# Performance work log

Hardware: AMD Instinct MI355X
Metric: run time of the kernel (lower is better)

## Reference

```python
import jax, jax.numpy as jnp
import numpy as np

N = 2048
E = 32768
IN_CH = 512
HID = 64
HEADS = 4
OUT_CH = 64
NUM_HOPS = 2
BETA = 0.5
NEG_SLOPE = 0.2
LN_EPS = 1e-5


def setup_inputs() -> dict:
    key = jax.random.key(0)
    ks = jax.random.split(key, 12)
    x = jax.random.normal(ks[0], (N, IN_CH), jnp.float32)
    edge_index = jax.random.randint(ks[1], (2, E), 0, N, dtype=jnp.int32)
    g = lambda k, shape, fan_in: jax.random.normal(k, shape, jnp.float32) * (1.0 / np.sqrt(fan_in))
    return {
        'x': x,
        'edge_index': edge_index,
        'l1_lin_w': g(ks[2], (NUM_HOPS, IN_CH, HEADS * HID), IN_CH),
        'l1_att_src': g(ks[3], (NUM_HOPS, HEADS, HID), HID),
        'l1_att_dst': g(ks[4], (NUM_HOPS, HEADS, HID), HID),
        'l1_hop_att': jnp.ones((NUM_HOPS,), jnp.float32),
        'l1_bias': g(ks[5], (HEADS * HID,), HEADS * HID),
        'l2_lin_w': g(ks[6], (NUM_HOPS, HEADS * HID, OUT_CH), HEADS * HID),
        'l2_att_src': g(ks[7], (NUM_HOPS, 1, OUT_CH), OUT_CH),
        'l2_att_dst': g(ks[8], (NUM_HOPS, 1, OUT_CH), OUT_CH),
        'l2_hop_att': jnp.ones((NUM_HOPS,), jnp.float32),
        'l2_res_w': g(ks[9], (HEADS * HID, OUT_CH), HEADS * HID),
        'l2_ln_scale': jnp.ones((OUT_CH,), jnp.float32),
        'l2_ln_bias': jnp.zeros((OUT_CH,), jnp.float32),
        'l2_bias': g(ks[10], (OUT_CH,), OUT_CH),
    }


def _leaky(v):
    return jnp.where(v >= 0, v, NEG_SLOPE * v)


def _masked_softmax_src(score, mask):
    # PyG softmax(alpha, edge_index[1]): normalize over src (axis 0) per dst column.
    s = jnp.where(mask[:, :, None], score, -jnp.inf)
    s = s - jnp.max(s, axis=0, keepdims=True)  # diag always valid -> finite max
    e = jnp.exp(s)
    return e / jnp.sum(e, axis=0, keepdims=True)


def _mgat_conv(x, A, motif, lin_w, att_src, att_dst, hop_att, heads, out_ch, concat,
               res_w=None, ln_scale=None, ln_bias=None, bias=None, residual=False):
    n = x.shape[0]
    hop_w = jax.nn.softmax(hop_att)
    eye = jnp.eye(n, dtype=bool)
    out = 0.0
    A_pow = A  # adj^(hop+1)
    for hop in range(NUM_HOPS):
        mask = (A_pow > 0) | eye  # remove_self_loops + add_self_loops -> diag always in
        hop_x = (x @ lin_w[hop]).reshape(n, heads, out_ch)
        s_src = jnp.einsum('nhc,hc->nh', hop_x, att_src[hop])
        s_dst = jnp.einsum('nhc,hc->nh', hop_x, att_dst[hop])
        score = s_src[:, None, :] + s_dst[None, :, :]  # [src, dst, h]
        a_first = _masked_softmax_src(_leaky(score), mask)
        a_motif = _masked_softmax_src(_leaky(score * motif[:, :, None]), mask)
        alpha = BETA * a_first + (1.0 - BETA) * a_motif
        hop_out = jnp.einsum('sdh,shc->dhc', alpha, hop_x)  # scatter-add at dst
        out = out + hop_w[hop] * hop_out
        A_pow = A_pow @ A
    if concat:
        out = out.reshape(n, heads * out_ch)
    else:
        out = out.mean(axis=1)
    if residual:
        res = x @ res_w if res_w is not None else x
        out = out + res
        mu = jnp.mean(out, axis=-1, keepdims=True)
        var = jnp.mean((out - mu) ** 2, axis=-1, keepdims=True)
        out = (out - mu) / jnp.sqrt(var + LN_EPS) * ln_scale + ln_bias
    if bias is not None:
        out = out + bias
    return out


def reference(x, edge_index, l1_lin_w, l1_att_src, l1_att_dst, l1_hop_att, l1_bias,
              l2_lin_w, l2_att_src, l2_att_dst, l2_hop_att, l2_res_w,
              l2_ln_scale, l2_ln_bias, l2_bias):
    n = x.shape[0]
    A = jnp.zeros((n, n), x.dtype).at[edge_index[0], edge_index[1]].set(1.0)
    motif = A @ A @ A
    motif = motif / jnp.maximum(motif.sum(axis=-1, keepdims=True), 1.0)
    h = _mgat_conv(x, A, motif, l1_lin_w, l1_att_src, l1_att_dst, l1_hop_att,
                   heads=HEADS, out_ch=HID, concat=True, bias=l1_bias, residual=False)
    h = jax.nn.elu(h)  # dropout p in eval mode -> identity
    out = _mgat_conv(h, A, motif, l2_lin_w, l2_att_src, l2_att_dst, l2_hop_att,
                     heads=1, out_ch=OUT_CH, concat=False,
                     res_w=l2_res_w, ln_scale=l2_ln_scale, ln_bias=l2_ln_bias,
                     bias=l2_bias, residual=True)
    return out
```

## Files before the change

kernel.cpp:

```cpp
#include <hip/hip_runtime.h>

namespace {

constexpr int kN = 2048;
constexpr int kWords = kN / 64;
constexpr int kC1 = 256;
constexpr int kC2 = 64;
constexpr int kIN = 512;
constexpr float kNegSlope = 0.2f;
constexpr float kLnEps = 1e-5f;

__device__ __forceinline__ float leakyf(float v) {
  return v >= 0.f ? v : kNegSlope * v;
}
__device__ __forceinline__ void onl(float& m, float& l, float v) {
  if (v > m) { l = l * __expf(m - v) + 1.f; m = v; }
  else       { l += __expf(v - m); }
}
__device__ __forceinline__ void mergeml(float& M, float& L, float m, float l) {
  if (m > M) { L = L * __expf(M - m) + l; M = m; }
  else       { L += l * __expf(m - M); }
}

__global__ void build_bits(const int* __restrict__ ei, int E,
                           unsigned long long* rowbits, unsigned long long* colbitsT) {
  int e = blockIdx.x * 256 + threadIdx.x;
  if (e >= E) return;
  int s = ei[e], d = ei[E + e];
  atomicOr(&rowbits[(size_t)s * kWords + (d >> 6)], 1ull << (d & 63));
  atomicOr(&colbitsT[(size_t)(s >> 6) * kN + d], 1ull << (s & 63));
}

__global__ __launch_bounds__(256) void a2_tiled(
    const unsigned long long* __restrict__ rowbits,
    const unsigned long long* __restrict__ colbitsT,
    unsigned short* __restrict__ A2,
    unsigned long long* __restrict__ colbits2T) {
  int bx = blockIdx.x, by = blockIdx.y;
  int t = threadIdx.x;
  __shared__ unsigned long long rb[64][33];
  __shared__ unsigned long long cb[32][64];
  __shared__ unsigned long long cw[64];
  int s0 = by * 64, d0 = bx * 64;
  for (int i = t; i < 64 * 32; i += 256) {
    int ss = i >> 5, w = i & 31;
    rb[ss][w] = rowbits[(size_t)(s0 + ss) * kWords + w];
  }
  for (int i = t; i < 32 * 64; i += 256) {
    int w = i >> 6, dd = i & 63;
    cb[w][dd] = colbitsT[(size_t)w * kN + d0 + dd];
  }
  if (t < 64) cw[t] = 0ull;
  __syncthreads();
  int tx = t & 15, ty4 = (t >> 4) * 4;
  int acc[4][4] = {};
#pragma unroll 4
  for (int w = 0; w < 32; ++w) {
    unsigned long long r0 = rb[ty4 + 0][w], r1 = rb[ty4 + 1][w];
    unsigned long long r2 = rb[ty4 + 2][w], r3 = rb[ty4 + 3][w];
    unsigned long long c0 = cb[w][tx], c1 = cb[w][tx + 16];
    unsigned long long c2 = cb[w][tx + 32], c3 = cb[w][tx + 48];
    acc[0][0] += __popcll(r0 & c0); acc[0][1] += __popcll(r0 & c1);
    acc[0][2] += __popcll(r0 & c2); acc[0][3] += __popcll(r0 & c3);
    acc[1][0] += __popcll(r1 & c0); acc[1][1] += __popcll(r1 & c1);
    acc[1][2] += __popcll(r1 & c2); acc[1][3] += __popcll(r1 & c3);
    acc[2][0] += __popcll(r2 & c0); acc[2][1] += __popcll(r2 & c1);
    acc[2][2] += __popcll(r2 & c2); acc[2][3] += __popcll(r2 & c3);
    acc[3][0] += __popcll(r3 & c0); acc[3][1] += __popcll(r3 & c1);
    acc[3][2] += __popcll(r3 & c2); acc[3][3] += __popcll(r3 & c3);
  }
#pragma unroll
  for (int i = 0; i < 4; ++i)
#pragma unroll
    for (int j = 0; j < 4; ++j)
      A2[(size_t)(s0 + ty4 + i) * kN + d0 + tx + 16 * j] = (unsigned short)acc[i][j];
#pragma unroll
  for (int j = 0; j < 4; ++j) {
    unsigned long long m = 0;
#pragma unroll
    for (int i = 0; i < 4; ++i)
      if (acc[i][j]) m |= 1ull << (ty4 + i);
    if (m) atomicOr(&cw[tx + 16 * j], m);
  }
  __syncthreads();
  if (t < 64) colbits2T[(size_t)by * kN + d0 + t] = cw[t];
}

__global__ __launch_bounds__(256) void a3_dense(
    const unsigned long long* __restrict__ rowbits,
    const unsigned short* __restrict__ A2,
    unsigned short* __restrict__ a3u,
    float* __restrict__ invr) {
  int s = blockIdx.x;
  int t = threadIdx.x;
  int lane = t & 63;
  __shared__ unsigned short jl[kN];
  __shared__ int jtot_s;
  __shared__ float redv[4];
  if (t < 64) {
    unsigned long long word = (lane < kWords) ? rowbits[(size_t)s * kWords + lane] : 0ull;
    int c = __popcll(word);
    int inc = c;
    for (int o = 1; o < 64; o <<= 1) { int v = __shfl_up(inc, o); if (lane >= o) inc += v; }
    if (lane == 63) jtot_s = inc;
    int off = inc - c;
    int base = lane * 64;
    while (word) {
      int b = __builtin_ctzll(word);
      word &= word - 1;
      jl[off++] = (unsigned short)(base + b);
    }
  }
  __syncthreads();
  int jtot = jtot_s;
  const uint4* a2v = reinterpret_cast<const uint4*>(A2);
  uint4 acc = make_uint4(0u, 0u, 0u, 0u);
  int ji = 0;
  for (; ji + 4 <= jtot; ji += 4) {
    uint4 v0 = a2v[(size_t)jl[ji + 0] * 256 + t];
    uint4 v1 = a2v[(size_t)jl[ji + 1] * 256 + t];
    uint4 v2 = a2v[(size_t)jl[ji + 2] * 256 + t];
    uint4 v3 = a2v[(size_t)jl[ji + 3] * 256 + t];
    acc.x += v0.x + v1.x + v2.x + v3.x;
    acc.y += v0.y + v1.y + v2.y + v3.y;
    acc.z += v0.z + v1.z + v2.z + v3.z;
    acc.w += v0.w + v1.w + v2.w + v3.w;
  }
  for (; ji < jtot; ++ji) {
    uint4 v = a2v[(size_t)jl[ji] * 256 + t];
    acc.x += v.x; acc.y += v.y; acc.z += v.z; acc.w += v.w;
  }
  reinterpret_cast<uint4*>(a3u)[(size_t)s * 256 + t] = acc;
  float tot = (float)((acc.x & 0xffffu) + (acc.x >> 16) +
                      (acc.y & 0xffffu) + (acc.y >> 16) +
                      (acc.z & 0xffffu) + (acc.z >> 16) +
                      (acc.w & 0xffffu) + (acc.w >> 16));
  for (int o = 32; o; o >>= 1) tot += __shfl_xor(tot, o);
  if (lane == 0) redv[t >> 6] = tot;
  __syncthreads();
  if (t == 0)
    invr[s] = 1.f / fmaxf(redv[0] + redv[1] + redv[2] + redv[3], 1.f);
}

__global__ __launch_bounds__(256) void transpose_motif(
    const unsigned short* __restrict__ a3u, const float* __restrict__ invr,
    float* __restrict__ motifT) {
  __shared__ float tile[64][65];
  __shared__ float invs[64];
  int d0 = blockIdx.x * 64, s0 = blockIdx.y * 64;
  int t = threadIdx.x;
  int tx = t & 63, ty = t >> 6;
  if (t < 64) invs[t] = invr[s0 + t];
  __syncthreads();
#pragma unroll
  for (int i = 0; i < 64; i += 4)
    tile[ty + i][tx] = (float)a3u[(size_t)(s0 + ty + i) * kN + d0 + tx] * invs[ty + i];
  __syncthreads();
#pragma unroll
  for (int i = 0; i < 64; i += 4)
    motifT[(size_t)(d0 + ty + i) * kN + s0 + tx] = tile[tx][ty + i];
}

__global__ __launch_bounds__(256) void gemm1(
    const float* __restrict__ x, const float* __restrict__ l1w,
    float* __restrict__ hx1,
    const float* __restrict__ l1as, const float* __restrict__ l1ad,
    float* __restrict__ ss1, float* __restrict__ sd1) {
  int hop = blockIdx.z;
  int row0 = blockIdx.y * 32, col0 = blockIdx.x * 64;
  const float* B = l1w + (size_t)hop * kIN * kC1;
  float* Cz = hx1 + (size_t)hop * kN * kC1;
  __shared__ float As[16][34];
  __shared__ float Bs[16][65];
  int t = threadIdx.x;
  int tx = t & 15, ty = t >> 4;
  float acc[2][4] = {};
  for (int k0 = 0; k0 < kIN; k0 += 16) {
    if (t < 128) {
      int m = t >> 2, kk = (t & 3) * 4;
      float4 va = *reinterpret_cast<const float4*>(x + (size_t)(row0 + m) * kIN + k0 + kk);
      As[kk + 0][m] = va.x; As[kk + 1][m] = va.y;
      As[kk + 2][m] = va.z; As[kk + 3][m] = va.w;
    }
    {
      int kb = t >> 4, nb = (t & 15) * 4;
      float4 vb = *reinterpret_cast<const float4*>(B + (size_t)(k0 + kb) * kC1 + col0 + nb);
      Bs[kb][nb + 0] = vb.x; Bs[kb][nb + 1] = vb.y;
      Bs[kb][nb + 2] = vb.z; Bs[kb][nb + 3] = vb.w;
    }
    __syncthreads();
#pragma unroll
    for (int kk2 = 0; kk2 < 16; ++kk2) {
      float a0 = As[kk2][ty * 2 + 0];
      float a1 = As[kk2][ty * 2 + 1];
      float b[4];
#pragma unroll
      for (int j = 0; j < 4; ++j) b[j] = Bs[kk2][tx * 4 + j];
#pragma unroll
      for (int j = 0; j < 4; ++j) {
        acc[0][j] += a0 * b[j];
        acc[1][j] += a1 * b[j];
      }
    }
    __syncthreads();
  }
#pragma unroll
  for (int i = 0; i < 2; ++i)
#pragma unroll
    for (int j = 0; j < 4; ++j)
      Cz[(size_t)(row0 + ty * 2 + i) * kC1 + col0 + tx * 4 + j] = acc[i][j];
  int h = col0 >> 6;
  float as_[4], ad_[4];
#pragma unroll
  for (int j = 0; j < 4; ++j) {
    as_[j] = l1as[hop * kC1 + col0 + tx * 4 + j];
    ad_[j] = l1ad[hop * kC1 + col0 + tx * 4 + j];
  }
#pragma unroll
  for (int i = 0; i < 2; ++i) {
    float ps = acc[i][0] * as_[0] + acc[i][1] * as_[1] +
               acc[i][2] * as_[2] + acc[i][3] * as_[3];
    float pd = acc[i][0] * ad_[0] + acc[i][1] * ad_[1] +
               acc[i][2] * ad_[2] + acc[i][3] * ad_[3];
#pragma unroll
    for (int o = 1; o < 16; o <<= 1) {
      ps += __shfl_xor(ps, o);
      pd += __shfl_xor(pd, o);
    }
    if (tx == 0) {
      int n = row0 + ty * 2 + i;
      ss1[((size_t)hop * kN + n) * 4 + h] = ps;
      sd1[((size_t)hop * kN + n) * 4 + h] = pd;
    }
  }
}

__global__ __launch_bounds__(256) void gemm2(
    const float* __restrict__ A, const float* __restrict__ l2w,
    const float* __restrict__ l2rw, float* __restrict__ C,
    const float* __restrict__ attS, const float* __restrict__ attD,
    float* __restrict__ ssO, float* __restrict__ sdO) {
  int z = blockIdx.z;
  const float* B = (z < 2) ? l2w + (size_t)z * kC1 * kC2 : l2rw;
  float* Cz = C + (size_t)z * kN * kC2;
  __shared__ float As[16][34];
  __shared__ float Bs[16][65];
  int t = threadIdx.x;
  int tx = t & 15, ty = t >> 4;
  int row0 = blockIdx.y * 16;
  float acc[4] = {};
  for (int k0 = 0; k0 < kC1; k0 += 16) {
    if (t < 64) {
      int m = t >> 2, kk = (t & 3) * 4;
      float4 va = *reinterpret_cast<const float4*>(A + (size_t)(row0 + m) * kC1 + k0 + kk);
      As[kk + 0][m] = va.x; As[kk + 1][m] = va.y;
      As[kk + 2][m] = va.z; As[kk + 3][m] = va.w;
    }
    {
      int kb = t >> 4, nb = (t & 15) * 4;
      float4 vb = *reinterpret_cast<const float4*>(B + (size_t)(k0 + kb) * kC2 + nb);
      Bs[kb][nb + 0] = vb.x; Bs[kb][nb + 1] = vb.y;
      Bs[kb][nb + 2] = vb.z; Bs[kb][nb + 3] = vb.w;
    }
    __syncthreads();
#pragma unroll
    for (int kk2 = 0; kk2 < 16; ++kk2) {
      float a = As[kk2][ty];
#pragma unroll
      for (int j = 0; j < 4; ++j) acc[j] += a * Bs[kk2][tx * 4 + j];
    }
    __syncthreads();
  }
#pragma unroll
  for (int j = 0; j < 4; ++j)
    Cz[(size_t)(row0 + ty) * kC2 + tx * 4 + j] = acc[j];
  if (z < 2) {
    float as_[4], ad_[4];
#pragma unroll
    for (int j = 0; j < 4; ++j) {
      as_[j] = attS[z * kC2 + tx * 4 + j];
      ad_[j] = attD[z * kC2 + tx * 4 + j];
    }
    float ps = acc[0] * as_[0] + acc[1] * as_[1] + acc[2] * as_[2] + acc[3] * as_[3];
    float pd = acc[0] * ad_[0] + acc[1] * ad_[1] + acc[2] * ad_[2] + acc[3] * ad_[3];
#pragma unroll
    for (int o = 1; o < 16; o <<= 1) {
      ps += __shfl_xor(ps, o);
      pd += __shfl_xor(pd, o);
    }
    if (tx == 0) {
      int n = row0 + ty;
      ssO[(size_t)z * kN + n] = ps;
      sdO[(size_t)z * kN + n] = pd;
    }
  }
}

__global__ __launch_bounds__(256) void agg_l1(
    const float* __restrict__ hx,
    const float* __restrict__ ssrc,
    const float* __restrict__ sdst,
    const float* __restrict__ motifT,
    const unsigned long long* __restrict__ colbitsT,
    const unsigned long long* __restrict__ colbits2T,
    const float* __restrict__ hop_att,
    const float* __restrict__ bias,
    float* __restrict__ hbuf) {
  int d = blockIdx.x;
  int t = threadIdx.x;
  int lane = t & 63;
  int h = t >> 6;
  int cq = lane;
  int hq = cq >> 4;
  __shared__ unsigned short slist[kN];
  __shared__ float mrow[kN];
  __shared__ float w_lds[64 * 4];
  __shared__ int s_total;
  __shared__ float4 red4[4][64];
  {
    const float4* mp = reinterpret_cast<const float4*>(motifT + (size_t)d * kN);
    float4* mr = reinterpret_cast<float4*>(mrow);
    mr[t] = mp[t];
    mr[t + 256] = mp[t + 256];
  }
  float a0 = hop_att[0], a1 = hop_att[1];
  float mxa = fmaxf(a0, a1);
  float e0 = __expf(a0 - mxa), e1 = __expf(a1 - mxa);
  float wh0 = e0 / (e0 + e1), wh1 = e1 / (e0 + e1);
  float4 acc4 = make_float4(0.f, 0.f, 0.f, 0.f);
  for (int hop = 0; hop < 2; ++hop) {
    const unsigned long long* cm = hop ? colbits2T : colbitsT;
    if (t < 64) {
      unsigned long long word = (lane < kWords) ? cm[(size_t)lane * kN + d] : 0ull;
      if (lane == (d >> 6)) word |= 1ull << (d & 63);
      int cnt = __popcll(word);
      int inc = cnt;
      for (int o = 1; o < 64; o <<= 1) { int v = __shfl_up(inc, o); if (lane >= o) inc += v; }
      if (lane == 63) s_total = inc;
      int off = inc - cnt;
      int base = lane * 64;
      while (word) {
        int b = __builtin_ctzll(word);
        word &= word - 1;
        slist[off++] = (unsigned short)(base + b);
      }
    }
    __syncthreads();
    int total = s_total;
    float sd = sdst[((size_t)hop * kN + d) * 4 + h];
    const float4* hx4 = reinterpret_cast<const float4*>(hx + (size_t)hop * kN * kC1);
    const float* ssp = ssrc + (size_t)hop * kN * 4;
    float m1 = -3.0e38f, l1v = 0.f, m2 = -3.0e38f, l2v = 0.f;
    for (int q = lane; q < total; q += 64) {
      int s = slist[q];
      float mv = mrow[s];
      float v = ssp[s * 4 + h] + sd;
      onl(m1, l1v, leakyf(v));
      onl(m2, l2v, leakyf(v * mv));
    }
#pragma unroll
    for (int o = 1; o < 64; o <<= 1) {
      float mm = __shfl_xor(m1, o), ll = __shfl_xor(l1v, o);
      mergeml(m1, l1v, mm, ll);
      float mm2 = __shfl_xor(m2, o), ll2 = __shfl_xor(l2v, o);
      mergeml(m2, l2v, mm2, ll2);
    }
    float il1 = 1.f / l1v, il2 = 1.f / l2v;
    float wh = hop ? wh1 : wh0;
    for (int c0 = 0; c0 < total; c0 += 64) {
      int nsi = min(64, total - c0);
      if (lane < nsi) {
        int s = slist[c0 + lane];
        float mv = mrow[s];
        float v = ssp[s * 4 + h] + sd;
        w_lds[lane * 4 + h] = (0.5f * __expf(leakyf(v) - m1) * il1 +
                               0.5f * __expf(leakyf(v * mv) - m2) * il2) * wh;
      }
      __syncthreads();
      int q = h;
      for (; q + 4 < nsi; q += 8) {
        int s0 = slist[c0 + q], s1 = slist[c0 + q + 4];
        float4 r0 = hx4[(size_t)s0 * 64 + cq];
        float4 r1 = hx4[(size_t)s1 * 64 + cq];
        float w0 = w_lds[q * 4 + hq], w1 = w_lds[(q + 4) * 4 + hq];
        acc4.x += w0 * r0.x + w1 * r1.x;
        acc4.y += w0 * r0.y + w1 * r1.y;
        acc4.z += w0 * r0.z + w1 * r1.z;
        acc4.w += w0 * r0.w + w1 * r1.w;
      }
      if (q < nsi) {
        int s0 = slist[c0 + q];
        float4 r0 = hx4[(size_t)s0 * 64 + cq];
        float w0 = w_lds[q * 4 + hq];
        acc4.x += w0 * r0.x; acc4.y += w0 * r0.y;
        acc4.z += w0 * r0.z; acc4.w += w0 * r0.w;
      }
      __syncthreads();
    }
    __syncthreads();
  }
  red4[h][cq] = acc4;
  __syncthreads();
  if (t < 64) {
    float4 a = red4[0][t], b = red4[1][t], c = red4[2][t], e = red4[3][t];
    float4 bv = reinterpret_cast<const float4*>(bias)[t];
    float4 v;
    v.x = a.x + b.x + c.x + e.x + bv.x;
    v.y = a.y + b.y + c.y + e.y + bv.y;
    v.z = a.z + b.z + c.z + e.z + bv.z;
    v.w = a.w + b.w + c.w + e.w + bv.w;
    v.x = v.x > 0.f ? v.x : __expf(v.x) - 1.f;
    v.y = v.y > 0.f ? v.y : __expf(v.y) - 1.f;
    v.z = v.z > 0.f ? v.z : __expf(v.z) - 1.f;
    v.w = v.w > 0.f ? v.w : __expf(v.w) - 1.f;
    reinterpret_cast<float4*>(hbuf)[(size_t)d * 64 + t] = v;
  }
}

__global__ __launch_bounds__(256) void agg_l2(
    const float* __restrict__ hx,
    const float* __restrict__ ssrc,
    const float* __restrict__ sdst,
    const float* __restrict__ motifT,
    const unsigned long long* __restrict__ colbitsT,
    const unsigned long long* __restrict__ colbits2T,
    const float* __restrict__ hop_att,
    const float* __restrict__ res,
    const float* __restrict__ lns, const float* __restrict__ lnb,
    const float* __restrict__ l2b,
    float* __restrict__ out) {
  int d = blockIdx.x;
  int t = threadIdx.x;
  int lane = t & 63;
  int g = t >> 6;
  int cq = t & 15;
  int sg = t >> 4;
  __shared__ unsigned short slist[kN];
  __shared__ float mrow[kN];
  __shared__ float w_lds[64];
  __shared__ int s_total;
  __shared__ float4 red4[16][16];
  __shared__ float out_lds[64];
  __shared__ float smst[4][4];
  {
    const float4* mp = reinterpret_cast<const float4*>(motifT + (size_t)d * kN);
    float4* mr = reinterpret_cast<float4*>(mrow);
    mr[t] = mp[t];
    mr[t + 256] = mp[t + 256];
  }
  float a0 = hop_att[0], a1 = hop_att[1];
  float mxa = fmaxf(a0, a1);
  float e0 = __expf(a0 - mxa), e1 = __expf(a1 - mxa);
  float wh0 = e0 / (e0 + e1), wh1 = e1 / (e0 + e1);
  float4 acc4 = make_float4(0.f, 0.f, 0.f, 0.f);
  for (int hop = 0; hop < 2; ++hop) {
    const unsigned long long* cm = hop ? colbits2T : colbitsT;
    if (t < 64) {
      unsigned long long word = (lane < kWords) ? cm[(size_t)lane * kN + d] : 0ull;
      if (lane == (d >> 6)) word |= 1ull << (d & 63);
      int cnt = __popcll(word);
      int inc = cnt;
      for (int o = 1; o < 64; o <<= 1) { int v = __shfl_up(inc, o); if (lane >= o) inc += v; }
      if (lane == 63) s_total = inc;
      int off = inc - cnt;
      int base = lane * 64;
      while (word) {
        int b = __builtin_ctzll(word);
        word &= word - 1;
        slist[off++] = (unsigned short)(base + b);
      }
    }
    __syncthreads();
    int total = s_total;
    float sd = sdst[(size_t)hop * kN + d];
    const float4* hx4 = reinterpret_cast<const float4*>(hx + (size_t)hop * kN * kC2);
    const float* ssp = ssrc + (size_t)hop * kN;
    float m1 = -3.0e38f, l1v = 0.f, m2 = -3.0e38f, l2v = 0.f;
    for (int q = t; q < total; q += 256) {
      int s = slist[q];
      float mv = mrow[s];
      float v = ssp[s] + sd;
      onl(m1, l1v, leakyf(v));
      onl(m2, l2v, leakyf(v * mv));
    }
#pragma unroll
    for (int o = 1; o < 64; o <<= 1) {
      float mm = __shfl_xor(m1, o), ll = __shfl_xor(l1v, o);
      mergeml(m1, l1v, mm, ll);
      float mm2 = __shfl_xor(m2, o), ll2 = __shfl_xor(l2v, o);
      mergeml(m2, l2v, mm2, ll2);
    }
    if (lane == 0) {
      smst[g][0] = m1; smst[g][1] = l1v; smst[g][2] = m2; smst[g][3] = l2v;
    }
    __syncthreads();
    float M1 = -3.0e38f, L1 = 0.f, M2 = -3.0e38f, L2 = 0.f;
#pragma unroll
    for (int gg = 0; gg < 4; ++gg) {
      mergeml(M1, L1, smst[gg][0], smst[gg][1]);
      mergeml(M2, L2, smst[gg][2], smst[gg][3]);
    }
    float il1 = 1.f / L1, il2 = 1.f / L2;
    float wh = hop ? wh1 : wh0;
    for (int c0 = 0; c0 < total; c0 += 64) {
      int nsi = min(64, total - c0);
      if (t < nsi) {
        int s = slist[c0 + t];
        float mv = mrow[s];
        float v = ssp[s] + sd;
        w_lds[t] = (0.5f * __expf(leakyf(v) - M1) * il1 +
                    0.5f * __expf(leakyf(v * mv) - M2) * il2) * wh;
      }
      __syncthreads();
      int q = sg;
      for (; q + 16 < nsi; q += 32) {
        int s0 = slist[c0 + q], s1 = slist[c0 + q + 16];
        float4 r0 = hx4[(size_t)s0 * 16 + cq];
        float4 r1 = hx4[(size_t)s1 * 16 + cq];
        float w0 = w_lds[q], w1 = w_lds[q + 16];
        acc4.x += w0 * r0.x + w1 * r1.x;
        acc4.y += w0 * r0.y + w1 * r1.y;
        acc4.z += w0 * r0.z + w1 * r1.z;
        acc4.w += w0 * r0.w + w1 * r1.w;
      }
      if (q < nsi) {
        int s0 = slist[c0 + q];
        float4 r0 = hx4[(size_t)s0 * 16 + cq];
        float w0 = w_lds[q];
        acc4.x += w0 * r0.x; acc4.y += w0 * r0.y;
        acc4.z += w0 * r0.z; acc4.w += w0 * r0.w;
      }
      __syncthreads();
    }
    __syncthreads();
  }
  red4[sg][cq] = acc4;
  __syncthreads();
  if (t < 16) {
    float4 v = make_float4(0.f, 0.f, 0.f, 0.f);
#pragma unroll
    for (int q = 0; q < 16; ++q) {
      float4 a = red4[q][t];
      v.x += a.x; v.y += a.y; v.z += a.z; v.w += a.w;
    }
    out_lds[t * 4 + 0] = v.x;
    out_lds[t * 4 + 1] = v.y;
    out_lds[t * 4 + 2] = v.z;
    out_lds[t * 4 + 3] = v.w;
  }
  __syncthreads();
  if (t < 64) {
    float v = out_lds[t] + res[(size_t)d * kC2 + t];
    float s = v;
    for (int o = 32; o; o >>= 1) s += __shfl_xor(s, o);
    float mu = s * (1.f / kC2);
    float dv = v - mu;
    float q = dv * dv;
    for (int o = 32; o; o >>= 1) q += __shfl_xor(q, o);
    float var = q * (1.f / kC2);
    out[(size_t)d * kC2 + t] = dv * rsqrtf(var + kLnEps) * lns[t] + lnb[t] + l2b[t];
  }
}

}

extern "C" void kernel_launch(void* const* d_in, const int* in_sizes, int n_in,
                              void* d_out, int out_size, void* d_ws, size_t ws_size,
                              hipStream_t stream) {
  const float* x    = (const float*)d_in[0];
  const int*   ei   = (const int*)d_in[1];
  const float* l1w  = (const float*)d_in[2];
  const float* l1as = (const float*)d_in[3];
  const float* l1ad = (const float*)d_in[4];
  const float* l1ha = (const float*)d_in[5];
  const float* l1b  = (const float*)d_in[6];
  const float* l2w  = (const float*)d_in[7];
  const float* l2as = (const float*)d_in[8];
  const float* l2ad = (const float*)d_in[9];
  const float* l2ha = (const float*)d_in[10];
  const float* l2rw = (const float*)d_in[11];
  const float* lns  = (const float*)d_in[12];
  const float* lnb  = (const float*)d_in[13];
  const float* l2b  = (const float*)d_in[14];
  int E = in_sizes[1] / 2;

  size_t o = 0;
  auto take = [&](size_t bytes) { size_t r = o; o += (bytes + 255) & ~(size_t)255; return r; };
  size_t oRB  = take((size_t)kN * kWords * 8);
  size_t oCB  = take((size_t)kWords * kN * 8);
  size_t zEnd = o;
  size_t oCB2 = take((size_t)kWords * kN * 8);
  size_t oA2  = take((size_t)kN * kN * 2);
  size_t oA3  = take((size_t)kN * kN * 2);
  size_t oINV = take((size_t)kN * 4);
  size_t oMFT = take((size_t)kN * kN * 4);
  size_t oHX1 = take((size_t)2 * kN * kC1 * 4);
  size_t oH   = take((size_t)kN * kC1 * 4);
  size_t oHX2 = take((size_t)3 * kN * kC2 * 4);
  size_t oSS1 = take((size_t)2 * kN * 4 * 4);
  size_t oSD1 = take((size_t)2 * kN * 4 * 4);
  size_t oSS2 = take((size_t)2 * kN * 4);
  size_t oSD2 = take((size_t)2 * kN * 4);
  if (ws_size < o) return;

  char* w = (char*)d_ws;
  unsigned long long* rowbits = (unsigned long long*)(w + oRB);
  unsigned long long* colbitsT = (unsigned long long*)(w + oCB);
  unsigned long long* colbits2T = (unsigned long long*)(w + oCB2);
  unsigned short* A2 = (unsigned short*)(w + oA2);
  unsigned short* A3u = (unsigned short*)(w + oA3);
  float* invr = (float*)(w + oINV);
  float* motifT = (float*)(w + oMFT);
  float* hx1 = (float*)(w + oHX1);
  float* hbuf = (float*)(w + oH);
  float* hx2 = (float*)(w + oHX2);
  float* res = hx2 + (size_t)2 * kN * kC2;
  float* ss1 = (float*)(w + oSS1);
  float* sd1 = (float*)(w + oSD1);
  float* ss2 = (float*)(w + oSS2);
  float* sd2 = (float*)(w + oSD2);

  hipMemsetAsync(d_ws, 0, zEnd, stream);

  build_bits<<<(E + 255) / 256, 256, 0, stream>>>(ei, E, rowbits, colbitsT);
  a2_tiled<<<dim3(kN / 64, kN / 64), 256, 0, stream>>>(rowbits, colbitsT, A2, colbits2T);
  a3_dense<<<kN, 256, 0, stream>>>(rowbits, A2, A3u, invr);
  transpose_motif<<<dim3(kN / 64, kN / 64), 256, 0, stream>>>(A3u, invr, motifT);

  gemm1<<<dim3(kC1 / 64, kN / 32, 2), 256, 0, stream>>>(x, l1w, hx1, l1as, l1ad, ss1, sd1);
  agg_l1<<<kN, 256, 0, stream>>>(hx1, ss1, sd1, motifT, colbitsT, colbits2T,
                                 l1ha, l1b, hbuf);

  gemm2<<<dim3(1, kN / 16, 3), 256, 0, stream>>>(hbuf, l2w, l2rw, hx2,
                                                 l2as, l2ad, ss2, sd2);
  agg_l2<<<kN, 256, 0, stream>>>(hx2, ss2, sd2, motifT, colbitsT, colbits2T,
                                 l2ha, res, lns, lnb, l2b, (float*)d_out);
}
```

Baseline: 178.8 us.

## Double-buffer shared tiles and vectorize LDS access in gemm1/gemm2

Both small GEMM kernels now keep two shared-memory tiles. The next K-slice is prefetched into registers while the current slice is computed, which cuts the per-iteration barriers from two to one. A is stored row-major with float4 stores instead of being transposed scalar-by-scalar. B is read with float4 LDS loads, and results are written with float4 global stores. This hides global load latency and reduces LDS instruction count, at the cost of more shared memory and registers per block.

New measurement: 148.1 us (median of 2 runs). 17.2% less time.

```diff
diff --git a/kernel.cpp b/kernel.cpp
--- a/kernel.cpp
+++ b/kernel.cpp
@@ -170,45 +170,52 @@
   int row0 = blockIdx.y * 32, col0 = blockIdx.x * 64;
   const float* B = l1w + (size_t)hop * kIN * kC1;
   float* Cz = hx1 + (size_t)hop * kN * kC1;
-  __shared__ float As[16][34];
-  __shared__ float Bs[16][65];
+  __shared__ float As[2][32][20];
+  __shared__ float Bs[2][16][68];
   int t = threadIdx.x;
   int tx = t & 15, ty = t >> 4;
+  int am = t >> 2, ak = (t & 3) * 4;
+  int bk = t >> 4, bn = (t & 15) * 4;
+  float4 ra, rb;
+  if (t < 128)
+    ra = *reinterpret_cast<const float4*>(x + (size_t)(row0 + am) * kIN + ak);
+  rb = *reinterpret_cast<const float4*>(B + (size_t)bk * kC1 + col0 + bn);
+  if (t < 128)
+    *reinterpret_cast<float4*>(&As[0][am][ak]) = ra;
+  *reinterpret_cast<float4*>(&Bs[0][bk][bn]) = rb;
+  __syncthreads();
   float acc[2][4] = {};
-  for (int k0 = 0; k0 < kIN; k0 += 16) {
-    if (t < 128) {
-      int m = t >> 2, kk = (t & 3) * 4;
-      float4 va = *reinterpret_cast<const float4*>(x + (size_t)(row0 + m) * kIN + k0 + kk);
-      As[kk + 0][m] = va.x; As[kk + 1][m] = va.y;
-      As[kk + 2][m] = va.z; As[kk + 3][m] = va.w;
-    }
-    {
-      int kb = t >> 4, nb = (t & 15) * 4;
-      float4 vb = *reinterpret_cast<const float4*>(B + (size_t)(k0 + kb) * kC1 + col0 + nb);
-      Bs[kb][nb + 0] = vb.x; Bs[kb][nb + 1] = vb.y;
-      Bs[kb][nb + 2] = vb.z; Bs[kb][nb + 3] = vb.w;
-    }
-    __syncthreads();
-#pragma unroll
-    for (int kk2 = 0; kk2 < 16; ++kk2) {
-      float a0 = As[kk2][ty * 2 + 0];
-      float a1 = As[kk2][ty * 2 + 1];
-      float b[4];
-#pragma unroll
-      for (int j = 0; j < 4; ++j) b[j] = Bs[kk2][tx * 4 + j];
-#pragma unroll
-      for (int j = 0; j < 4; ++j) {
-        acc[0][j] += a0 * b[j];
-        acc[1][j] += a1 * b[j];
-      }
-    }
-    __syncthreads();
-  }
-#pragma unroll
-  for (int i = 0; i < 2; ++i)
-#pragma unroll
-    for (int j = 0; j < 4; ++j)
-      Cz[(size_t)(row0 + ty * 2 + i) * kC1 + col0 + tx * 4 + j] = acc[i][j];
+  int cur = 0;
+  for (int k0 = 16; k0 <= kIN; k0 += 16) {
+    bool more = (k0 < kIN);
+    if (more) {
+      if (t < 128)
+        ra = *reinterpret_cast<const float4*>(x + (size_t)(row0 + am) * kIN + k0 + ak);
+      rb = *reinterpret_cast<const float4*>(B + (size_t)(k0 + bk) * kC1 + col0 + bn);
+    }
+#pragma unroll
+    for (int kk = 0; kk < 16; ++kk) {
+      float a0 = As[cur][ty * 2 + 0][kk];
+      float a1 = As[cur][ty * 2 + 1][kk];
+      float4 b = *reinterpret_cast<const float4*>(&Bs[cur][kk][tx * 4]);
+      acc[0][0] += a0 * b.x; acc[0][1] += a0 * b.y;
+      acc[0][2] += a0 * b.z; acc[0][3] += a0 * b.w;
+      acc[1][0] += a1 * b.x; acc[1][1] += a1 * b.y;
+      acc[1][2] += a1 * b.z; acc[1][3] += a1 * b.w;
+    }
+    if (more) {
+      if (t < 128)
+        *reinterpret_cast<float4*>(&As[cur ^ 1][am][ak]) = ra;
+      *reinterpret_cast<float4*>(&Bs[cur ^ 1][bk][bn]) = rb;
+      __syncthreads();
+      cur ^= 1;
+    }
+  }
+#pragma unroll
+  for (int i = 0; i < 2; ++i) {
+    float4 c = make_float4(acc[i][0], acc[i][1], acc[i][2], acc[i][3]);
+    *reinterpret_cast<float4*>(Cz + (size_t)(row0 + ty * 2 + i) * kC1 + col0 + tx * 4) = c;
+  }
   int h = col0 >> 6;
   float as_[4], ad_[4];
 #pragma unroll
@@ -243,37 +250,49 @@
   int z = blockIdx.z;
   const float* B = (z < 2) ? l2w + (size_t)z * kC1 * kC2 : l2rw;
   float* Cz = C + (size_t)z * kN * kC2;
-  __shared__ float As[16][34];
-  __shared__ float Bs[16][65];
+  __shared__ float As[2][16][20];
+  __shared__ float Bs[2][16][68];
   int t = threadIdx.x;
   int tx = t & 15, ty = t >> 4;
   int row0 = blockIdx.y * 16;
+  int am = t >> 2, ak = (t & 3) * 4;
+  int bk = t >> 4, bn = (t & 15) * 4;
+  float4 ra, rb;
+  if (t < 64)
+    ra = *reinterpret_cast<const float4*>(A + (size_t)(row0 + am) * kC1 + ak);
+  rb = *reinterpret_cast<const float4*>(B + (size_t)bk * kC2 + bn);
+  if (t < 64)
+    *reinterpret_cast<float4*>(&As[0][am][ak]) = ra;
+  *reinterpret_cast<float4*>(&Bs[0][bk][bn]) = rb;
+  __syncthreads();
   float acc[4] = {};
-  for (int k0 = 0; k0 < kC1; k0 += 16) {
-    if (t < 64) {
-      int m = t >> 2, kk = (t & 3) * 4;
-      float4 va = *reinterpret_cast<const float4*>(A + (size_t)(row0 + m) * kC1 + k0 + kk);
-      As[kk + 0][m] = va.x; As[kk + 1][m] = va.y;
-      As[kk + 2][m] = va.z; As[kk + 3][m] = va.w;
-    }
-    {
-      int kb = t >> 4, nb = (t & 15) * 4;
-      float4 vb = *reinterpret_cast<const float4*>(B + (size_t)(k0 + kb) * kC2 + nb);
-      Bs[kb][nb + 0] = vb.x; Bs[kb][nb + 1] = vb.y;
-      Bs[kb][nb + 2] = vb.z; Bs[kb][nb + 3] = vb.w;
-    }
-    __syncthreads();
-#pragma unroll
-    for (int kk2 = 0; kk2 < 16; ++kk2) {
-      float a = As[kk2][ty];
-#pragma unroll
-      for (int j = 0; j < 4; ++j) acc[j] += a * Bs[kk2][tx * 4 + j];
-    }
-    __syncthreads();
-  }
-#pragma unroll
-  for (int j = 0; j < 4; ++j)
-    Cz[(size_t)(row0 + ty) * kC2 + tx * 4 + j] = acc[j];
+  int cur = 0;
+  for (int k0 = 16; k0 <= kC1; k0 += 16) {
+    bool more = (k0 < kC1);
+    if (more) {
+      if (t < 64)
+        ra = *reinterpret_cast<const float4*>(A + (size_t)(row0 + am) * kC1 + k0 + ak);
+      rb = *reinterpret_cast<const float4*>(B + (size_t)(k0 + bk) * kC2 + bn);
+    }
+#pragma unroll
+    for (int kk = 0; kk < 16; ++kk) {
+      float a = As[cur][ty][kk];
+      float4 b = *reinterpret_cast<const float4*>(&Bs[cur][kk][tx * 4]);
+      acc[0] += a * b.x; acc[1] += a * b.y;
+      acc[2] += a * b.z; acc[3] += a * b.w;
+    }
+    if (more) {
+      if (t < 64)
+        *reinterpret_cast<float4*>(&As[cur ^ 1][am][ak]) = ra;
+      *reinterpret_cast<float4*>(&Bs[cur ^ 1][bk][bn]) = rb;
+      __syncthreads();
+      cur ^= 1;
+    }
+  }
+  {
+    float4 c = make_float4(acc[0], acc[1], acc[2], acc[3]);
+    *reinterpret_cast<float4*>(Cz + (size_t)(row0 + ty) * kC2 + tx * 4) = c;
+  }
   if (z < 2) {
     float as_[4], ad_[4];
 #pragma unroll
```
